# Performance work log

Measured on AMD Instinct MI355X. Metric: run time of the kernel, lower is better.

## Reference

```python
import jax, jax.numpy as jnp
import numpy as np

CELL_DIM = 64
FIELD_SIZE = 1.0

def setup_inputs() -> dict:
    key = jax.random.key(0)
    k1, k2 = jax.random.split(key)
    x = jax.random.normal(k1, (8192, CELL_DIM), dtype=jnp.float32)
    placeCells = jax.random.normal(k2, (512, CELL_DIM), dtype=jnp.float32)
    return {"x": x, "placeCells": placeCells}

def reference(x, placeCells):
    # states: (N, cellDim)
    states = x.reshape(-1, CELL_DIM)
    # broadcast L1 distance to every codebook cell: (N, numCells)
    l1 = jnp.sum(jnp.abs(states[:, None, :] - placeCells[None, :, :]), axis=-1)
    dists_squared = l1 * l1
    unnormalized = -dists_squared / (2.0 * FIELD_SIZE * FIELD_SIZE)
    return jax.nn.softmax(unnormalized, axis=1)
```

## Files before the change

### kernel.cpp

```cpp
#include <hip/hip_runtime.h>

#define DIM    64
#define NCELLS 512
#define CHUNK  256
#define ROWS_PER_BLOCK 16
#define NROWS  8192

__global__ __launch_bounds__(256, 2)
void placecells_kernel(const float* __restrict__ x,
                       const float* __restrict__ pc,
                       float* __restrict__ out)
{
    __shared__ float pcT[DIM * CHUNK];

    const int tid = (int)threadIdx.x;
    const int l   = tid & 63;
    const int w   = __builtin_amdgcn_readfirstlane(tid >> 6);
    const int rowBase = (int)blockIdx.x * ROWS_PER_BLOCK + w * 4;

    float4 d00{0,0,0,0}, d10{0,0,0,0}, d20{0,0,0,0}, d30{0,0,0,0};
    float4 d01{0,0,0,0}, d11{0,0,0,0}, d21{0,0,0,0}, d31{0,0,0,0};

    auto do_chunk = [&](int ch, float4& a0, float4& a1, float4& a2, float4& a3) {
        #pragma unroll 4
        for (int i = 0; i < 16; ++i) {
            int idx = i * 256 + tid;
            int cl  = idx >> 4;
            int k4  = idx & 15;
            float4 v = *(const float4*)(pc + (ch * CHUNK + cl) * DIM + k4 * 4);
            int pq = (cl >> 2) ^ k4;
            float* p = &pcT[(k4 * 4) * CHUNK + pq * 4 + (cl & 3)];
            p[0 * CHUNK] = v.x;
            p[1 * CHUNK] = v.y;
            p[2 * CHUNK] = v.z;
            p[3 * CHUNK] = v.w;
        }
        __syncthreads();

        #pragma unroll 4
        for (int k4 = 0; k4 < 16; ++k4) {
            float4 xv0 = *(const float4*)(x + (rowBase + 0) * DIM + k4 * 4);
            float4 xv1 = *(const float4*)(x + (rowBase + 1) * DIM + k4 * 4);
            float4 xv2 = *(const float4*)(x + (rowBase + 2) * DIM + k4 * 4);
            float4 xv3 = *(const float4*)(x + (rowBase + 3) * DIM + k4 * 4);
            const int pq4 = (l ^ k4) * 4;
            #pragma unroll
            for (int j = 0; j < 4; ++j) {
                float4 pv = *(const float4*)(&pcT[(k4 * 4 + j) * CHUNK + pq4]);
                float x0 = (j == 0) ? xv0.x : (j == 1) ? xv0.y : (j == 2) ? xv0.z : xv0.w;
                float x1 = (j == 0) ? xv1.x : (j == 1) ? xv1.y : (j == 2) ? xv1.z : xv1.w;
                float x2 = (j == 0) ? xv2.x : (j == 1) ? xv2.y : (j == 2) ? xv2.z : xv2.w;
                float x3 = (j == 0) ? xv3.x : (j == 1) ? xv3.y : (j == 2) ? xv3.z : xv3.w;
                a0.x += fabsf(x0 - pv.x); a0.y += fabsf(x0 - pv.y);
                a0.z += fabsf(x0 - pv.z); a0.w += fabsf(x0 - pv.w);
                a1.x += fabsf(x1 - pv.x); a1.y += fabsf(x1 - pv.y);
                a1.z += fabsf(x1 - pv.z); a1.w += fabsf(x1 - pv.w);
                a2.x += fabsf(x2 - pv.x); a2.y += fabsf(x2 - pv.y);
                a2.z += fabsf(x2 - pv.z); a2.w += fabsf(x2 - pv.w);
                a3.x += fabsf(x3 - pv.x); a3.y += fabsf(x3 - pv.y);
                a3.z += fabsf(x3 - pv.z); a3.w += fabsf(x3 - pv.w);
            }
        }
    };

    do_chunk(0, d00, d10, d20, d30);
    __syncthreads();
    do_chunk(1, d01, d11, d21, d31);

    auto finish_row = [&](float4 a, float4 b, int r) {
        float mn = fminf(fminf(fminf(a.x, a.y), fminf(a.z, a.w)),
                         fminf(fminf(b.x, b.y), fminf(b.z, b.w)));
        #pragma unroll
        for (int off = 32; off > 0; off >>= 1)
            mn = fminf(mn, __shfl_xor(mn, off, 64));
        float m2 = mn * mn;

        float e0 = __expf(0.5f * (m2 - a.x * a.x));
        float e1 = __expf(0.5f * (m2 - a.y * a.y));
        float e2 = __expf(0.5f * (m2 - a.z * a.z));
        float e3 = __expf(0.5f * (m2 - a.w * a.w));
        float e4 = __expf(0.5f * (m2 - b.x * b.x));
        float e5 = __expf(0.5f * (m2 - b.y * b.y));
        float e6 = __expf(0.5f * (m2 - b.z * b.z));
        float e7 = __expf(0.5f * (m2 - b.w * b.w));
        float s = ((e0 + e1) + (e2 + e3)) + ((e4 + e5) + (e6 + e7));
        #pragma unroll
        for (int off = 32; off > 0; off >>= 1)
            s += __shfl_xor(s, off, 64);
        float inv = 1.0f / s;

        float* orow = out + (size_t)(rowBase + r) * NCELLS;
        *(float4*)(orow + 4 * l)         = make_float4(e0 * inv, e1 * inv, e2 * inv, e3 * inv);
        *(float4*)(orow + CHUNK + 4 * l) = make_float4(e4 * inv, e5 * inv, e6 * inv, e7 * inv);
    };
    finish_row(d00, d01, 0);
    finish_row(d10, d11, 1);
    finish_row(d20, d21, 2);
    finish_row(d30, d31, 3);
}

extern "C" void kernel_launch(void* const* d_in, const int* in_sizes, int n_in,
                              void* d_out, int out_size, void* d_ws, size_t ws_size,
                              hipStream_t stream)
{
    const float* x  = (const float*)d_in[0];
    const float* pc = (const float*)d_in[1];
    float* out = (float*)d_out;
    placecells_kernel<<<dim3(NROWS / ROWS_PER_BLOCK), dim3(256), 0, stream>>>(x, pc, out);
}
```

Before: 81.27 us.

## Split K dimension into shared-memory chunks and halve rows per block for occupancy

Shared-memory staging of the codebook now covers 32 of the 64 feature dimensions at a time (32 KB instead of 64 KB), done in four stage/compute phases. Each wave now handles 2 rows instead of 4, so blocks cover 8 rows, the grid doubles, and launch bounds ask for 4 blocks per CU. The aim is higher occupancy and latency hiding. In exchange each block stages the whole codebook for half as many rows, which doubles codebook traffic per output row and adds more barriers.

```diff
diff --git a/kernel.cpp b/kernel.cpp
--- a/kernel.cpp
+++ b/kernel.cpp
@@ -2,70 +2,69 @@
 
 #define DIM    64
 #define NCELLS 512
-#define CHUNK  256
-#define ROWS_PER_BLOCK 16
+#define CC     256
+#define KC     32
+#define ROWS_PER_BLOCK 8
 #define NROWS  8192
 
-__global__ __launch_bounds__(256, 2)
+__global__ __launch_bounds__(256, 4)
 void placecells_kernel(const float* __restrict__ x,
                        const float* __restrict__ pc,
                        float* __restrict__ out)
 {
-    __shared__ float pcT[DIM * CHUNK];
+    __shared__ float pcT[KC * CC];
 
     const int tid = (int)threadIdx.x;
     const int l   = tid & 63;
     const int w   = __builtin_amdgcn_readfirstlane(tid >> 6);
-    const int rowBase = (int)blockIdx.x * ROWS_PER_BLOCK + w * 4;
+    const int rowBase = (int)blockIdx.x * ROWS_PER_BLOCK + w * 2;
 
-    float4 d00{0,0,0,0}, d10{0,0,0,0}, d20{0,0,0,0}, d30{0,0,0,0};
-    float4 d01{0,0,0,0}, d11{0,0,0,0}, d21{0,0,0,0}, d31{0,0,0,0};
+    float4 a00{0,0,0,0}, a10{0,0,0,0};
+    float4 a01{0,0,0,0}, a11{0,0,0,0};
 
-    auto do_chunk = [&](int ch, float4& a0, float4& a1, float4& a2, float4& a3) {
-        #pragma unroll 4
-        for (int i = 0; i < 16; ++i) {
+    auto stage = [&](int cc, int kc) {
+        #pragma unroll
+        for (int i = 0; i < 8; ++i) {
             int idx = i * 256 + tid;
-            int cl  = idx >> 4;
-            int k4  = idx & 15;
-            float4 v = *(const float4*)(pc + (ch * CHUNK + cl) * DIM + k4 * 4);
+            int cl  = idx >> 3;
+            int k4  = idx & 7;
+            float4 v = *(const float4*)(pc + (cc * CC + cl) * DIM + kc * KC + k4 * 4);
             int pq = (cl >> 2) ^ k4;
-            float* p = &pcT[(k4 * 4) * CHUNK + pq * 4 + (cl & 3)];
-            p[0 * CHUNK] = v.x;
-            p[1 * CHUNK] = v.y;
-            p[2 * CHUNK] = v.z;
-            p[3 * CHUNK] = v.w;
+            float* p = &pcT[(k4 * 4) * CC + pq * 4 + (cl & 3)];
+            p[0 * CC] = v.x;
+            p[1 * CC] = v.y;
+            p[2 * CC] = v.z;
+            p[3 * CC] = v.w;
         }
-        __syncthreads();
+    };
 
-        #pragma unroll 4
-        for (int k4 = 0; k4 < 16; ++k4) {
-            float4 xv0 = *(const float4*)(x + (rowBase + 0) * DIM + k4 * 4);
-            float4 xv1 = *(const float4*)(x + (rowBase + 1) * DIM + k4 * 4);
-            float4 xv2 = *(const float4*)(x + (rowBase + 2) * DIM + k4 * 4);
-            float4 xv3 = *(const float4*)(x + (rowBase + 3) * DIM + k4 * 4);
+    auto compute = [&](int kc, float4& A0, float4& A1) {
+        #pragma unroll
+        for (int k4 = 0; k4 < 8; ++k4) {
+            float4 xv0 = *(const float4*)(x + (rowBase + 0) * DIM + kc * KC + k4 * 4);
+            float4 xv1 = *(const float4*)(x + (rowBase + 1) * DIM + kc * KC + k4 * 4);
             const int pq4 = (l ^ k4) * 4;
             #pragma unroll
             for (int j = 0; j < 4; ++j) {
-                float4 pv = *(const float4*)(&pcT[(k4 * 4 + j) * CHUNK + pq4]);
+                float4 pv = *(const float4*)(&pcT[(k4 * 4 + j) * CC + pq4]);
                 float x0 = (j == 0) ? xv0.x : (j == 1) ? xv0.y : (j == 2) ? xv0.z : xv0.w;
                 float x1 = (j == 0) ? xv1.x : (j == 1) ? xv1.y : (j == 2) ? xv1.z : xv1.w;
-                float x2 = (j == 0) ? xv2.x : (j == 1) ? xv2.y : (j == 2) ? xv2.z : xv2.w;
-                float x3 = (j == 0) ? xv3.x : (j == 1) ? xv3.y : (j == 2) ? xv3.z : xv3.w;
-                a0.x += fabsf(x0 - pv.x); a0.y += fabsf(x0 - pv.y);
-                a0.z += fabsf(x0 - pv.z); a0.w += fabsf(x0 - pv.w);
-                a1.x += fabsf(x1 - pv.x); a1.y += fabsf(x1 - pv.y);
-                a1.z += fabsf(x1 - pv.z); a1.w += fabsf(x1 - pv.w);
-                a2.x += fabsf(x2 - pv.x); a2.y += fabsf(x2 - pv.y);
-                a2.z += fabsf(x2 - pv.z); a2.w += fabsf(x2 - pv.w);
-                a3.x += fabsf(x3 - pv.x); a3.y += fabsf(x3 - pv.y);
-                a3.z += fabsf(x3 - pv.z); a3.w += fabsf(x3 - pv.w);
+                A0.x += fabsf(x0 - pv.x); A0.y += fabsf(x0 - pv.y);
+                A0.z += fabsf(x0 - pv.z); A0.w += fabsf(x0 - pv.w);
+                A1.x += fabsf(x1 - pv.x); A1.y += fabsf(x1 - pv.y);
+                A1.z += fabsf(x1 - pv.z); A1.w += fabsf(x1 - pv.w);
             }
         }
     };
 
-    do_chunk(0, d00, d10, d20, d30);
-    __syncthreads();
-    do_chunk(1, d01, d11, d21, d31);
+    stage(0, 0); __syncthreads();
+    compute(0, a00, a10);
+    __syncthreads(); stage(0, 1); __syncthreads();
+    compute(1, a00, a10);
+    __syncthreads(); stage(1, 0); __syncthreads();
+    compute(0, a01, a11);
+    __syncthreads(); stage(1, 1); __syncthreads();
+    compute(1, a01, a11);
 
     auto finish_row = [&](float4 a, float4 b, int r) {
         float mn = fminf(fminf(fminf(a.x, a.y), fminf(a.z, a.w)),
@@ -90,13 +89,11 @@
         float inv = 1.0f / s;
 
         float* orow = out + (size_t)(rowBase + r) * NCELLS;
-        *(float4*)(orow + 4 * l)         = make_float4(e0 * inv, e1 * inv, e2 * inv, e3 * inv);
-        *(float4*)(orow + CHUNK + 4 * l) = make_float4(e4 * inv, e5 * inv, e6 * inv, e7 * inv);
+        *(float4*)(orow + 4 * l)      = make_float4(e0 * inv, e1 * inv, e2 * inv, e3 * inv);
+        *(float4*)(orow + CC + 4 * l) = make_float4(e4 * inv, e5 * inv, e6 * inv, e7 * inv);
     };
-    finish_row(d00, d01, 0);
-    finish_row(d10, d11, 1);
-    finish_row(d20, d21, 2);
-    finish_row(d30, d31, 3);
+    finish_row(a00, a01, 0);
+    finish_row(a10, a11, 1);
 }
 
 extern "C" void kernel_launch(void* const* d_in, const int* in_sizes, int n_in,
```

New measurement: 81.29 us. About the same (+0.0%).

## Stage full codebook once per 1024-thread block, split cells across wave pairs

Applied to the files above, without the earlier changes.

The kernel now loads the whole 512x64 codebook into LDS (128KB) in one pass with a rotation-based bank swizzle, instead of two 256-cell chunks. Blocks grow to 1024 threads covering 32 rows, and each pair of waves splits the 512 cells of a row, so each thread keeps 4 accumulators instead of 8. Row min and sum are combined across the two waves through small LDS buffers with extra block barriers. The aim is to cut register pressure and remove the chunk reload barrier. The cost is a large LDS footprint that likely allows only one block per CU, and more block-wide synchronisation.

```diff
diff --git a/kernel.cpp b/kernel.cpp
--- a/kernel.cpp
+++ b/kernel.cpp
@@ -1,102 +1,136 @@
 #include <hip/hip_runtime.h>
 
+#define NCELLS 512
 #define DIM    64
-#define NCELLS 512
-#define CHUNK  256
-#define ROWS_PER_BLOCK 16
+#define ROWS_PER_BLOCK 32
 #define NROWS  8192
 
-__global__ __launch_bounds__(256, 2)
+__global__ __launch_bounds__(1024, 4)
 void placecells_kernel(const float* __restrict__ x,
                        const float* __restrict__ pc,
                        float* __restrict__ out)
 {
-    __shared__ float pcT[DIM * CHUNK];
+    __shared__ float pcT[DIM * NCELLS];
+    __shared__ float redMin[64];
+    __shared__ float redSum[64];
 
     const int tid = (int)threadIdx.x;
     const int l   = tid & 63;
-    const int w   = __builtin_amdgcn_readfirstlane(tid >> 6);
-    const int rowBase = (int)blockIdx.x * ROWS_PER_BLOCK + w * 4;
+    const int L   = tid & 127;
+    const int w1  = (tid >> 6) & 1;
+    const int p   = __builtin_amdgcn_readfirstlane(tid >> 7);
+    const int rowBase = (int)blockIdx.x * ROWS_PER_BLOCK + p * 4;
 
-    float4 d00{0,0,0,0}, d10{0,0,0,0}, d20{0,0,0,0}, d30{0,0,0,0};
-    float4 d01{0,0,0,0}, d11{0,0,0,0}, d21{0,0,0,0}, d31{0,0,0,0};
+    #pragma unroll
+    for (int i = 0; i < 8; ++i) {
+        int idx = i * 1024 + tid;
+        int cl  = idx & 511;
+        int k4  = idx >> 9;
+        float4 v = *(const float4*)(pc + cl * DIM + k4 * 4);
+        int k0 = k4 * 4;
+        pcT[(k0 + 0) * NCELLS + ((cl + 4 * (k0 + 0)) & 511)] = v.x;
+        pcT[(k0 + 1) * NCELLS + ((cl + 4 * (k0 + 1)) & 511)] = v.y;
+        pcT[(k0 + 2) * NCELLS + ((cl + 4 * (k0 + 2)) & 511)] = v.z;
+        pcT[(k0 + 3) * NCELLS + ((cl + 4 * (k0 + 3)) & 511)] = v.w;
+    }
+    __syncthreads();
 
-    auto do_chunk = [&](int ch, float4& a0, float4& a1, float4& a2, float4& a3) {
-        #pragma unroll 4
-        for (int i = 0; i < 16; ++i) {
-            int idx = i * 256 + tid;
-            int cl  = idx >> 4;
-            int k4  = idx & 15;
-            float4 v = *(const float4*)(pc + (ch * CHUNK + cl) * DIM + k4 * 4);
-            int pq = (cl >> 2) ^ k4;
-            float* p = &pcT[(k4 * 4) * CHUNK + pq * 4 + (cl & 3)];
-            p[0 * CHUNK] = v.x;
-            p[1 * CHUNK] = v.y;
-            p[2 * CHUNK] = v.z;
-            p[3 * CHUNK] = v.w;
+    float4 a0{0,0,0,0}, a1{0,0,0,0}, a2{0,0,0,0}, a3{0,0,0,0};
+
+    #pragma unroll 4
+    for (int k4 = 0; k4 < 16; ++k4) {
+        float4 xv0 = *(const float4*)(x + (rowBase + 0) * DIM + k4 * 4);
+        float4 xv1 = *(const float4*)(x + (rowBase + 1) * DIM + k4 * 4);
+        float4 xv2 = *(const float4*)(x + (rowBase + 2) * DIM + k4 * 4);
+        float4 xv3 = *(const float4*)(x + (rowBase + 3) * DIM + k4 * 4);
+        #pragma unroll
+        for (int j = 0; j < 4; ++j) {
+            const int k = k4 * 4 + j;
+            float4 pv = *(const float4*)(&pcT[k * NCELLS + ((4 * L + 4 * k) & 511)]);
+            float x0 = (j == 0) ? xv0.x : (j == 1) ? xv0.y : (j == 2) ? xv0.z : xv0.w;
+            float x1 = (j == 0) ? xv1.x : (j == 1) ? xv1.y : (j == 2) ? xv1.z : xv1.w;
+            float x2 = (j == 0) ? xv2.x : (j == 1) ? xv2.y : (j == 2) ? xv2.z : xv2.w;
+            float x3 = (j == 0) ? xv3.x : (j == 1) ? xv3.y : (j == 2) ? xv3.z : xv3.w;
+            a0.x += fabsf(x0 - pv.x); a0.y += fabsf(x0 - pv.y);
+            a0.z += fabsf(x0 - pv.z); a0.w += fabsf(x0 - pv.w);
+            a1.x += fabsf(x1 - pv.x); a1.y += fabsf(x1 - pv.y);
+            a1.z += fabsf(x1 - pv.z); a1.w += fabsf(x1 - pv.w);
+            a2.x += fabsf(x2 - pv.x); a2.y += fabsf(x2 - pv.y);
+            a2.z += fabsf(x2 - pv.z); a2.w += fabsf(x2 - pv.w);
+            a3.x += fabsf(x3 - pv.x); a3.y += fabsf(x3 - pv.y);
+            a3.z += fabsf(x3 - pv.z); a3.w += fabsf(x3 - pv.w);
         }
-        __syncthreads();
+    }
 
-        #pragma unroll 4
-        for (int k4 = 0; k4 < 16; ++k4) {
-            float4 xv0 = *(const float4*)(x + (rowBase + 0) * DIM + k4 * 4);
-            float4 xv1 = *(const float4*)(x + (rowBase + 1) * DIM + k4 * 4);
-            float4 xv2 = *(const float4*)(x + (rowBase + 2) * DIM + k4 * 4);
-            float4 xv3 = *(const float4*)(x + (rowBase + 3) * DIM + k4 * 4);
-            const int pq4 = (l ^ k4) * 4;
-            #pragma unroll
-            for (int j = 0; j < 4; ++j) {
-                float4 pv = *(const float4*)(&pcT[(k4 * 4 + j) * CHUNK + pq4]);
-                float x0 = (j == 0) ? xv0.x : (j == 1) ? xv0.y : (j == 2) ? xv0.z : xv0.w;
-                float x1 = (j == 0) ? xv1.x : (j == 1) ? xv1.y : (j == 2) ? xv1.z : xv1.w;
-                float x2 = (j == 0) ? xv2.x : (j == 1) ? xv2.y : (j == 2) ? xv2.z : xv2.w;
-                float x3 = (j == 0) ? xv3.x : (j == 1) ? xv3.y : (j == 2) ? xv3.z : xv3.w;
-                a0.x += fabsf(x0 - pv.x); a0.y += fabsf(x0 - pv.y);
-                a0.z += fabsf(x0 - pv.z); a0.w += fabsf(x0 - pv.w);
-                a1.x += fabsf(x1 - pv.x); a1.y += fabsf(x1 - pv.y);
-                a1.z += fabsf(x1 - pv.z); a1.w += fabsf(x1 - pv.w);
-                a2.x += fabsf(x2 - pv.x); a2.y += fabsf(x2 - pv.y);
-                a2.z += fabsf(x2 - pv.z); a2.w += fabsf(x2 - pv.w);
-                a3.x += fabsf(x3 - pv.x); a3.y += fabsf(x3 - pv.y);
-                a3.z += fabsf(x3 - pv.z); a3.w += fabsf(x3 - pv.w);
-            }
-        }
+    auto wmin = [&](float v) {
+        #pragma unroll
+        for (int off = 32; off > 0; off >>= 1) v = fminf(v, __shfl_xor(v, off, 64));
+        return v;
+    };
+    auto wsum = [&](float v) {
+        #pragma unroll
+        for (int off = 32; off > 0; off >>= 1) v += __shfl_xor(v, off, 64);
+        return v;
     };
 
-    do_chunk(0, d00, d10, d20, d30);
+    float m0 = wmin(fminf(fminf(a0.x, a0.y), fminf(a0.z, a0.w)));
+    float m1 = wmin(fminf(fminf(a1.x, a1.y), fminf(a1.z, a1.w)));
+    float m2 = wmin(fminf(fminf(a2.x, a2.y), fminf(a2.z, a2.w)));
+    float m3 = wmin(fminf(fminf(a3.x, a3.y), fminf(a3.z, a3.w)));
+    if (l == 0) {
+        redMin[p * 8 + w1 * 4 + 0] = m0;
+        redMin[p * 8 + w1 * 4 + 1] = m1;
+        redMin[p * 8 + w1 * 4 + 2] = m2;
+        redMin[p * 8 + w1 * 4 + 3] = m3;
+    }
     __syncthreads();
-    do_chunk(1, d01, d11, d21, d31);
+    float M0 = fminf(redMin[p * 8 + 0], redMin[p * 8 + 4 + 0]);
+    float M1 = fminf(redMin[p * 8 + 1], redMin[p * 8 + 4 + 1]);
+    float M2 = fminf(redMin[p * 8 + 2], redMin[p * 8 + 4 + 2]);
+    float M3 = fminf(redMin[p * 8 + 3], redMin[p * 8 + 4 + 3]);
 
-    auto finish_row = [&](float4 a, float4 b, int r) {
-        float mn = fminf(fminf(fminf(a.x, a.y), fminf(a.z, a.w)),
-                         fminf(fminf(b.x, b.y), fminf(b.z, b.w)));
-        #pragma unroll
-        for (int off = 32; off > 0; off >>= 1)
-            mn = fminf(mn, __shfl_xor(mn, off, 64));
-        float m2 = mn * mn;
+    float M0s = M0 * M0, M1s = M1 * M1, M2s = M2 * M2, M3s = M3 * M3;
+    float e00 = __expf(0.5f * (M0s - a0.x * a0.x));
+    float e01 = __expf(0.5f * (M0s - a0.y * a0.y));
+    float e02 = __expf(0.5f * (M0s - a0.z * a0.z));
+    float e03 = __expf(0.5f * (M0s - a0.w * a0.w));
+    float e10 = __expf(0.5f * (M1s - a1.x * a1.x));
+    float e11 = __expf(0.5f * (M1s - a1.y * a1.y));
+    float e12 = __expf(0.5f * (M1s - a1.z * a1.z));
+    float e13 = __expf(0.5f * (M1s - a1.w * a1.w));
+    float e20 = __expf(0.5f * (M2s - a2.x * a2.x));
+    float e21 = __expf(0.5f * (M2s - a2.y * a2.y));
+    float e22 = __expf(0.5f * (M2s - a2.z * a2.z));
+    float e23 = __expf(0.5f * (M2s - a2.w * a2.w));
+    float e30 = __expf(0.5f * (M3s - a3.x * a3.x));
+    float e31 = __expf(0.5f * (M3s - a3.y * a3.y));
+    float e32 = __expf(0.5f * (M3s - a3.z * a3.z));
+    float e33 = __expf(0.5f * (M3s - a3.w * a3.w));
 
-        float e0 = __expf(0.5f * (m2 - a.x * a.x));
-        float e1 = __expf(0.5f * (m2 - a.y * a.y));
-        float e2 = __expf(0.5f * (m2 - a.z * a.z));
-        float e3 = __expf(0.5f * (m2 - a.w * a.w));
-        float e4 = __expf(0.5f * (m2 - b.x * b.x));
-        float e5 = __expf(0.5f * (m2 - b.y * b.y));
-        float e6 = __expf(0.5f * (m2 - b.z * b.z));
-        float e7 = __expf(0.5f * (m2 - b.w * b.w));
-        float s = ((e0 + e1) + (e2 + e3)) + ((e4 + e5) + (e6 + e7));
-        #pragma unroll
-        for (int off = 32; off > 0; off >>= 1)
-            s += __shfl_xor(s, off, 64);
-        float inv = 1.0f / s;
+    float s0 = wsum((e00 + e01) + (e02 + e03));
+    float s1 = wsum((e10 + e11) + (e12 + e13));
+    float s2 = wsum((e20 + e21) + (e22 + e23));
+    float s3 = wsum((e30 + e31) + (e32 + e33));
+    if (l == 0) {
+        redSum[p * 8 + w1 * 4 + 0] = s0;
+        redSum[p * 8 + w1 * 4 + 1] = s1;
+        redSum[p * 8 + w1 * 4 + 2] = s2;
+        redSum[p * 8 + w1 * 4 + 3] = s3;
+    }
+    __syncthreads();
+    float i0 = 1.0f / (redSum[p * 8 + 0] + redSum[p * 8 + 4 + 0]);
+    float i1 = 1.0f / (redSum[p * 8 + 1] + redSum[p * 8 + 4 + 1]);
+    float i2 = 1.0f / (redSum[p * 8 + 2] + redSum[p * 8 + 4 + 2]);
+    float i3 = 1.0f / (redSum[p * 8 + 3] + redSum[p * 8 + 4 + 3]);
 
-        float* orow = out + (size_t)(rowBase + r) * NCELLS;
-        *(float4*)(orow + 4 * l)         = make_float4(e0 * inv, e1 * inv, e2 * inv, e3 * inv);
-        *(float4*)(orow + CHUNK + 4 * l) = make_float4(e4 * inv, e5 * inv, e6 * inv, e7 * inv);
-    };
-    finish_row(d00, d01, 0);
-    finish_row(d10, d11, 1);
-    finish_row(d20, d21, 2);
-    finish_row(d30, d31, 3);
+    float* o0 = out + (size_t)(rowBase + 0) * NCELLS + 4 * L;
+    float* o1 = out + (size_t)(rowBase + 1) * NCELLS + 4 * L;
+    float* o2 = out + (size_t)(rowBase + 2) * NCELLS + 4 * L;
+    float* o3 = out + (size_t)(rowBase + 3) * NCELLS + 4 * L;
+    *(float4*)o0 = make_float4(e00 * i0, e01 * i0, e02 * i0, e03 * i0);
+    *(float4*)o1 = make_float4(e10 * i1, e11 * i1, e12 * i1, e13 * i1);
+    *(float4*)o2 = make_float4(e20 * i2, e21 * i2, e22 * i2, e23 * i2);
+    *(float4*)o3 = make_float4(e30 * i3, e31 * i3, e32 * i3, e33 * i3);
 }
 
 extern "C" void kernel_launch(void* const* d_in, const int* in_sizes, int n_in,
@@ -106,5 +140,5 @@
     const float* x  = (const float*)d_in[0];
     const float* pc = (const float*)d_in[1];
     float* out = (float*)d_out;
-    placecells_kernel<<<dim3(NROWS / ROWS_PER_BLOCK), dim3(256), 0, stream>>>(x, pc, out);
+    placecells_kernel<<<dim3(NROWS / ROWS_PER_BLOCK), dim3(1024), 0, stream>>>(x, pc, out);
 }
```

Result: slower. 83.94 us (+3.3%).
